# Kernel optimization log

Measured on AMD Instinct MI355X. Metric: run time of the kernel, lower is better.

The kernel has to match this reference:

```python
import jax, jax.numpy as jnp
import numpy as np

N_EMBD = 1024
BLOCK_SIZE = 2048
B = 8
LN_EPS = 1e-5


def _mlp(x, W1, b1, W2, b2):
    # Linear -> exact GELU -> Linear (torch nn.GELU default is erf-based)
    h = jax.nn.gelu(x @ W1 + b1, approximate=False)
    return h @ W2 + b2


def setup_inputs() -> dict:
    key = jax.random.key(0)
    ks = jax.random.split(key, 14)
    C = N_EMBD
    std = 0.02
    d = {"x": jax.random.normal(ks[0], (B, BLOCK_SIZE, C), dtype=jnp.float32)}
    names = ["q", "k", "v"]
    i = 1
    for n in names:
        d[f"W1{n}"] = jax.random.normal(ks[i], (C, C), dtype=jnp.float32) * std; i += 1
        d[f"b1{n}"] = jnp.zeros((C,), dtype=jnp.float32)
        d[f"W2{n}"] = jax.random.normal(ks[i], (C, C), dtype=jnp.float32) * std; i += 1
        d[f"b2{n}"] = jnp.zeros((C,), dtype=jnp.float32)
    d["ln_w"] = jnp.ones((C,), dtype=jnp.float32)
    d["ln_b"] = jnp.zeros((C,), dtype=jnp.float32)
    return d


def reference(x, W1q, b1q, W2q, b2q, W1k, b1k, W2k, b2k, W1v, b1v, W2v, b2v, ln_w, ln_b):
    Bsz, T, C = x.shape
    q = _mlp(x, W1q, b1q, W2q, b2q)
    k = _mlp(x, W1k, b1k, W2k, b2k)
    v = _mlp(x, W1v, b1v, W2v, b2v)
    scale = np.sqrt(N_EMBD * BLOCK_SIZE).astype(np.float32)
    scores = jnp.einsum("bid,bjd->bij", q, k) / scale  # [B,T,T]
    mask = jnp.tril(jnp.ones((T, T), dtype=scores.dtype))
    scores = scores * mask
    out = jnp.einsum("bij,bjd->bid", scores, v)  # [B,T,C]
    # LayerNorm with weight+bias, eps=1e-5
    mu = jnp.mean(out, axis=-1, keepdims=True)
    var = jnp.mean(jnp.square(out - mu), axis=-1, keepdims=True)
    out = (out - mu) * jax.lax.rsqrt(var + LN_EPS) * ln_w + ln_b
    return out
```

## Files before the change

### kernel.cpp

```cpp
#include <hip/hip_runtime.h>
#include <math.h>

#define BM 128
#define BN 128
#define BK 64

typedef _Float16 f16x8 __attribute__((ext_vector_type(8)));
typedef __attribute__((ext_vector_type(4))) float f32x4;

typedef const __attribute__((address_space(1))) void* gas_ptr;
typedef __attribute__((address_space(3))) void* las_ptr;

enum { OP_NONE = 0, OP_BIAS_GELU = 1, OP_BIAS = 2, OP_SCALE_MASK = 3 };

__device__ __forceinline__ unsigned short f2h(float f) {
    _Float16 h = (_Float16)f;
    unsigned short u;
    __builtin_memcpy(&u, &h, 2);
    return u;
}
__device__ __forceinline__ float h2f(unsigned short u) {
    _Float16 h;
    __builtin_memcpy(&h, &u, 2);
    return (float)h;
}

__device__ __forceinline__ float fast_gelu(float x) {
    float x2 = x * x;
    float p  = x * (-1.5957691216f - 0.0713548164f * x2);
    float t  = __expf(p);
    return x * __builtin_amdgcn_rcpf(1.0f + t);
}

template <int EPI, bool CAUSAL_K, bool TRI, bool REVM>
__global__ __launch_bounds__(256, 4) void gemm_bt(
    const unsigned short* __restrict__ A,
    const unsigned short* __restrict__ BT,
    unsigned short* __restrict__ Cw,
    const float* __restrict__ bias0,
    const float* __restrict__ bias1,
    const float* __restrict__ bias2,
    int M, int N, int K,
    long long sA, long long sB, long long sC,
    float scale)
{
    __shared__ __align__(16) unsigned short As[BM * BK];
    __shared__ __align__(16) unsigned short Bs[BN * BK];

    const int tid  = threadIdx.x;
    const int wave = tid >> 6;
    const int lane = tid & 63;

    int bm, bn, z;
    if (TRI) {
        const int t = blockIdx.x;
        int i = (int)((sqrtf(8.0f * t + 1.0f) - 1.0f) * 0.5f);
        while ((i + 1) * (i + 2) / 2 <= t) i++;
        while (i * (i + 1) / 2 > t) i--;
        const int j = t - i * (i + 1) / 2;
        bm = i * BM;
        bn = j * BN;
        z  = blockIdx.y;
    } else {
        bm = (REVM ? (gridDim.x - 1 - blockIdx.x) : blockIdx.x) * BM;
        bn = blockIdx.y * BN;
        z  = blockIdx.z;
    }

    const unsigned short* Ab = A  + (long long)z * sA;
    const unsigned short* Bb = BT + (long long)z * sB;
    unsigned short*       Cb = Cw + (long long)z * sC;
    const float* bias = nullptr;
    if (EPI == OP_BIAS || EPI == OP_BIAS_GELU)
        bias = (z == 0) ? bias0 : (z == 1) ? bias1 : bias2;

    const int wm = (wave >> 1) * 64;
    const int wn = (wave & 1) * 64;

    f32x4 acc[4][4];
    #pragma unroll
    for (int i = 0; i < 4; i++)
        #pragma unroll
        for (int j = 0; j < 4; j++)
            acc[i][j] = (f32x4){0.f, 0.f, 0.f, 0.f};

    int Keff = K;
    if (CAUSAL_K) {
        int kl = bm + BM;
        Keff = kl < K ? kl : K;
    }

    const int srow = lane >> 3;
    const int gchw = ((lane & 7) ^ (srow & 7)) * 8;
    const int fr   = lane & 15;
    const int quad = lane >> 4;

    const unsigned short* pA = Ab + (long long)(bm + wave * 32 + srow) * K + gchw;
    const unsigned short* pB = Bb + (long long)(bn + wave * 32 + srow) * K + gchw;
    const long long rstep = 8ll * K;

    for (int k0 = 0; k0 < Keff; k0 += BK) {
        #pragma unroll
        for (int s = 0; s < 4; ++s) {
            const int t = wave * 4 + s;
            __builtin_amdgcn_global_load_lds((gas_ptr)(const void*)(pA + s * rstep),
                                             (las_ptr)(void*)&As[t * 512 + lane * 8],
                                             16, 0, 0);
            __builtin_amdgcn_global_load_lds((gas_ptr)(const void*)(pB + s * rstep),
                                             (las_ptr)(void*)&Bs[t * 512 + lane * 8],
                                             16, 0, 0);
        }
        pA += BK;
        pB += BK;
        __syncthreads();

        #pragma unroll
        for (int kk = 0; kk < 2; ++kk) {
            f16x8 fa[4], fb[4];
            #pragma unroll
            for (int i = 0; i < 4; i++) {
                const int row  = wm + i * 16 + fr;
                const int slot = row * 8 + ((kk * 4 + quad) ^ (fr & 7));
                fa[i] = *(const f16x8*)&As[slot * 8];
            }
            #pragma unroll
            for (int j = 0; j < 4; j++) {
                const int row  = wn + j * 16 + fr;
                const int slot = row * 8 + ((kk * 4 + quad) ^ (fr & 7));
                fb[j] = *(const f16x8*)&Bs[slot * 8];
            }
            #pragma unroll
            for (int i = 0; i < 4; i++)
                #pragma unroll
                for (int j = 0; j < 4; j++)
                    acc[i][j] = __builtin_amdgcn_mfma_f32_16x16x32_f16(
                        fa[i], fb[j], acc[i][j], 0, 0, 0);
        }
        __syncthreads();
    }

    const int er = quad;
    const int ec = fr;
    #pragma unroll
    for (int j = 0; j < 4; j++) {
        const int col = bn + wn + j * 16 + ec;
        float bj = 0.f;
        if (EPI == OP_BIAS || EPI == OP_BIAS_GELU) bj = bias[col];
        #pragma unroll
        for (int i = 0; i < 4; i++) {
            #pragma unroll
            for (int r = 0; r < 4; r++) {
                const int row = bm + wm + i * 16 + er * 4 + r;
                float v = acc[i][j][r];
                if (EPI == OP_BIAS_GELU) {
                    v = fast_gelu(v + bj);
                } else if (EPI == OP_BIAS) {
                    v += bj;
                } else if (EPI == OP_SCALE_MASK) {
                    v *= scale;
                    if (col > row) v = 0.f;
                }
                Cb[(long long)row * N + col] = f2h(v);
            }
        }
    }
}

__global__ __launch_bounds__(256) void cvt_f32_f16(
    const float4* __restrict__ in, ushort4* __restrict__ out)
{
    int i = blockIdx.x * 256 + threadIdx.x;
    float4 f = in[i];
    ushort4 o;
    o.x = f2h(f.x); o.y = f2h(f.y); o.z = f2h(f.z); o.w = f2h(f.w);
    out[i] = o;
}

__global__ __launch_bounds__(256) void wprep(
    const float* __restrict__ s0, const float* __restrict__ s1,
    const float* __restrict__ s2, const float* __restrict__ s3,
    const float* __restrict__ s4, const float* __restrict__ s5,
    unsigned short* __restrict__ W1T, unsigned short* __restrict__ W2T)
{
    const int C = 1024;
    const int z = blockIdx.z;
    const float* in = (z == 0) ? s0 : (z == 1) ? s1 : (z == 2) ? s2
                    : (z == 3) ? s3 : (z == 4) ? s4 : s5;
    unsigned short* out = (z < 3) ? (W1T + (long long)z * C * C)
                                  : (W2T + (long long)(z - 3) * C * C);
    __shared__ unsigned short tile[32][33];
    const int bx = blockIdx.x * 32;
    const int by = blockIdx.y * 32;
    const int x = threadIdx.x;
    for (int y = threadIdx.y; y < 32; y += 8)
        tile[y][x] = f2h(in[(long long)(by + y) * C + (bx + x)]);
    __syncthreads();
    for (int y = threadIdx.y; y < 32; y += 8)
        out[(long long)(bx + y) * C + (by + x)] = tile[x][y];
}

__global__ __launch_bounds__(256) void transpose64_f16(
    const unsigned short* __restrict__ in,
    unsigned short* __restrict__ out,
    int rows, int cols,
    long long sIn, long long sOut)
{
    __shared__ unsigned short tile[64][68];
    const unsigned short* ip = in  + (long long)blockIdx.z * sIn;
    unsigned short*       op = out + (long long)blockIdx.z * sOut;
    const int bx = blockIdx.x * 64;
    const int by = blockIdx.y * 64;
    const int tid = threadIdx.x;
    const int rsub = tid >> 4;
    const int c4   = (tid & 15) * 4;
    #pragma unroll
    for (int it = 0; it < 4; it++) {
        const int r = it * 16 + rsub;
        ushort4 v = *(const ushort4*)&ip[(long long)(by + r) * cols + (bx + c4)];
        tile[r][c4]     = v.x;
        tile[r][c4 + 1] = v.y;
        tile[r][c4 + 2] = v.z;
        tile[r][c4 + 3] = v.w;
    }
    __syncthreads();
    #pragma unroll
    for (int it = 0; it < 4; it++) {
        const int cc = it * 16 + rsub;
        ushort4 v;
        v.x = tile[c4][cc];
        v.y = tile[c4 + 1][cc];
        v.z = tile[c4 + 2][cc];
        v.w = tile[c4 + 3][cc];
        *(ushort4*)&op[(long long)(bx + cc) * rows + (by + c4)] = v;
    }
}

__global__ __launch_bounds__(256) void layernorm_h(
    const unsigned short* __restrict__ X,
    const float* __restrict__ W,
    const float* __restrict__ Bv,
    float* __restrict__ Y)
{
    const int row = blockIdx.x;
    const int tid = threadIdx.x;
    ushort4 u = ((const ushort4*)(X + (long long)row * 1024))[tid];
    float f0 = h2f(u.x), f1 = h2f(u.y), f2 = h2f(u.z), f3 = h2f(u.w);
    float s  = f0 + f1 + f2 + f3;
    float ss = f0 * f0 + f1 * f1 + f2 * f2 + f3 * f3;
    #pragma unroll
    for (int off = 32; off > 0; off >>= 1) {
        s  += __shfl_down(s, off);
        ss += __shfl_down(ss, off);
    }
    __shared__ float red[2][4];
    const int wv = tid >> 6;
    if ((tid & 63) == 0) { red[0][wv] = s; red[1][wv] = ss; }
    __syncthreads();
    float S  = red[0][0] + red[0][1] + red[0][2] + red[0][3];
    float SS = red[1][0] + red[1][1] + red[1][2] + red[1][3];
    float mu  = S * (1.f / 1024.f);
    float var = SS * (1.f / 1024.f) - mu * mu;
    float rs  = rsqrtf(var + 1e-5f);
    float4 w4 = ((const float4*)W)[tid];
    float4 b4 = ((const float4*)Bv)[tid];
    float4 o;
    o.x = (f0 - mu) * rs * w4.x + b4.x;
    o.y = (f1 - mu) * rs * w4.y + b4.y;
    o.z = (f2 - mu) * rs * w4.z + b4.z;
    o.w = (f3 - mu) * rs * w4.w + b4.w;
    ((float4*)(Y + (long long)row * 1024))[tid] = o;
}

extern "C" void kernel_launch(void* const* d_in, const int* in_sizes, int n_in,
                              void* d_out, int out_size, void* d_ws, size_t ws_size,
                              hipStream_t stream)
{
    const int C  = 1024;
    const int T  = 2048;
    const int NB = 8;
    const int MT = NB * T;

    const float* x = (const float*)d_in[0];
    const float* W1q = (const float*)d_in[1];
    const float* b1q = (const float*)d_in[2];
    const float* W2q = (const float*)d_in[3];
    const float* b2q = (const float*)d_in[4];
    const float* W1k = (const float*)d_in[5];
    const float* b1k = (const float*)d_in[6];
    const float* W2k = (const float*)d_in[7];
    const float* b2k = (const float*)d_in[8];
    const float* W1v = (const float*)d_in[9];
    const float* b1v = (const float*)d_in[10];
    const float* W2v = (const float*)d_in[11];
    const float* b2v = (const float*)d_in[12];
    const float* lnw = (const float*)d_in[13];
    const float* lnb = (const float*)d_in[14];

    char* wsp = (char*)d_ws;
    auto take = [&](size_t bytes) {
        char* p = wsp;
        wsp += (bytes + 255) & ~(size_t)255;
        return p;
    };

    const size_t MATE = (size_t)MT * C;

    unsigned short* W1T  = (unsigned short*)take((size_t)3 * C * C * 2);
    unsigned short* W2T  = (unsigned short*)take((size_t)3 * C * C * 2);
    unsigned short* xb   = (unsigned short*)take(MATE * 2);
    unsigned short* qkv  = (unsigned short*)take(3 * MATE * 2);
    unsigned short* hreg = (unsigned short*)take(3 * MATE * 2);
    unsigned short* qb   = qkv;
    unsigned short* kb   = qkv + MATE;
    unsigned short* vb   = qkv + 2 * MATE;
    unsigned short* vT   = xb;
    unsigned short* scb  = hreg;
    unsigned short* opre = hreg + (size_t)NB * T * T;

    cvt_f32_f16<<<dim3(MT * C / 1024, 1, 1), dim3(256, 1, 1), 0, stream>>>(
        (const float4*)x, (ushort4*)xb);

    wprep<<<dim3(C / 32, C / 32, 6), dim3(32, 8, 1), 0, stream>>>(
        W1q, W1k, W1v, W2q, W2k, W2v, W1T, W2T);

    dim3 blk(256, 1, 1);

    gemm_bt<OP_BIAS_GELU, false, false, false><<<dim3(MT / BM, C / BN, 3), blk, 0, stream>>>(
        xb, W1T, hreg, b1q, b1k, b1v, MT, C, C,
        0, (long long)C * C, (long long)MATE, 1.f);

    gemm_bt<OP_BIAS, false, false, false><<<dim3(MT / BM, C / BN, 3), blk, 0, stream>>>(
        hreg, W2T, qkv, b2q, b2k, b2v, MT, C, C,
        (long long)MATE, (long long)C * C, (long long)MATE, 1.f);

    transpose64_f16<<<dim3(C / 64, T / 64, NB), blk, 0, stream>>>(
        vb, vT, T, C, (long long)T * C, (long long)T * C);

    float inv_scale = 1.0f / sqrtf((float)C * (float)T);
    gemm_bt<OP_SCALE_MASK, false, true, false><<<dim3(136, NB, 1), blk, 0, stream>>>(
        qb, kb, scb, nullptr, nullptr, nullptr, T, T, C,
        (long long)T * C, (long long)T * C, (long long)T * T, inv_scale);

    gemm_bt<OP_NONE, true, false, true><<<dim3(T / BM, C / BN, NB), blk, 0, stream>>>(
        scb, vT, opre, nullptr, nullptr, nullptr, T, C, T,
        (long long)T * T, (long long)T * C, (long long)T * C, 1.f);

    layernorm_h<<<dim3(MT, 1, 1), dim3(256, 1, 1), 0, stream>>>(
        opre, lnw, lnb, (float*)d_out);
}
```

Baseline: 553.0 us.

## Use 256x256 double-buffered GEMM kernel for the QKV MLP projections

Adds a new 512-thread GEMM kernel with 256x256 output tiles, double-buffered LDS filled via global_load_lds, XOR-swizzled LDS layout, and interleaved load/MFMA phases with priority hints. It replaces the 128x128 kernel for the two MLP GEMMs. The larger tile raises arithmetic intensity and the pipeline overlaps loads with MFMA work. The cost is higher LDS (128KB) and register pressure, which limits occupancy, and only 768 blocks per launch.

New measurement: 584.7 us. +5.7%, slower.

```diff
diff --git a/kernel.cpp b/kernel.cpp
--- a/kernel.cpp
+++ b/kernel.cpp
@@ -30,6 +30,179 @@
     float p  = x * (-1.5957691216f - 0.0713548164f * x2);
     float t  = __expf(p);
     return x * __builtin_amdgcn_rcpf(1.0f + t);
+}
+
+template <int EPI>
+__global__ __launch_bounds__(512, 2) void gemm256(
+    const unsigned short* __restrict__ A,
+    const unsigned short* __restrict__ BT,
+    unsigned short* __restrict__ Cw,
+    const float* __restrict__ bias0,
+    const float* __restrict__ bias1,
+    const float* __restrict__ bias2,
+    int M, int N, int K,
+    long long sA, long long sB, long long sC)
+{
+    __shared__ __align__(16) unsigned short As[2 * 256 * 64];
+    __shared__ __align__(16) unsigned short Bs[2 * 256 * 64];
+
+    const int tid  = threadIdx.x;
+    const int wave = tid >> 6;
+    const int lane = tid & 63;
+
+    const int bm = blockIdx.x * 256;
+    const int bn = blockIdx.y * 256;
+    const int z  = blockIdx.z;
+
+    const unsigned short* Ab = A  + (long long)z * sA;
+    const unsigned short* Bb = BT + (long long)z * sB;
+    unsigned short*       Cb = Cw + (long long)z * sC;
+    const float* bias = (z == 0) ? bias0 : (z == 1) ? bias1 : bias2;
+
+    const int wm = (wave >> 2) * 128;
+    const int wn = (wave & 3) * 64;
+
+    const int srow = lane >> 3;
+    const int swzc = (lane & 7) ^ srow;
+    const int fr   = lane & 15;
+    const int quad = lane >> 4;
+
+    const unsigned short* srcA = Ab + (long long)(bm + wave * 8 + srow) * K + swzc * 8;
+    const unsigned short* srcB = Bb + (long long)(bn + wave * 8 + srow) * K + swzc * 8;
+
+    const int NT = K >> 6;
+    const int NI = NT >> 1;
+
+    f32x4 acc[8][4];
+    #pragma unroll
+    for (int i = 0; i < 8; i++)
+        #pragma unroll
+        for (int j = 0; j < 4; j++)
+            acc[i][j] = (f32x4){0.f, 0.f, 0.f, 0.f};
+
+#define STG(src, lds, t, h)                                                    \
+    {                                                                          \
+        const int tc_ = ((t) < NT) ? (t) : ((t) & 1);                          \
+        const int bs_ = ((t) & 1) * 16384;                                     \
+        _Pragma("unroll")                                                      \
+        for (int s_ = 0; s_ < 2; ++s_) {                                       \
+            __builtin_amdgcn_global_load_lds(                                  \
+                (gas_ptr)(const void*)((src) +                                 \
+                    (long long)((h) * 128 + s_ * 64) * K + tc_ * 64),          \
+                (las_ptr)(void*)&lds[bs_ +                                     \
+                    ((h) * 128 + s_ * 64 + wave * 8) * 64 + lane * 8],         \
+                16, 0, 0);                                                     \
+        }                                                                      \
+    }
+
+#define LDA(d, q)                                                              \
+    _Pragma("unroll")                                                          \
+    for (int i_ = 0; i_ < 2; ++i_) {                                           \
+        _Pragma("unroll")                                                      \
+        for (int kk_ = 0; kk_ < 2; ++kk_) {                                    \
+            const int row_ = wm + (q) * 32 + i_ * 16 + fr;                     \
+            const int sl_  = row_ * 8 + ((kk_ * 4 + quad) ^ (row_ & 7));       \
+            fa[i_][kk_] = *(const f16x8*)&As[(d) * 16384 + sl_ * 8];           \
+        }                                                                      \
+    }
+
+#define LDB(d)                                                                 \
+    _Pragma("unroll")                                                          \
+    for (int j_ = 0; j_ < 4; ++j_) {                                           \
+        _Pragma("unroll")                                                      \
+        for (int kk_ = 0; kk_ < 2; ++kk_) {                                    \
+            const int row_ = wn + j_ * 16 + fr;                                \
+            const int sl_  = row_ * 8 + ((kk_ * 4 + quad) ^ (row_ & 7));       \
+            fb[j_][kk_] = *(const f16x8*)&Bs[(d) * 16384 + sl_ * 8];           \
+        }                                                                      \
+    }
+
+#define MFMAQ(q)                                                               \
+    __builtin_amdgcn_s_setprio(1);                                             \
+    _Pragma("unroll")                                                          \
+    for (int kk_ = 0; kk_ < 2; ++kk_) {                                        \
+        _Pragma("unroll")                                                      \
+        for (int i_ = 0; i_ < 2; ++i_) {                                       \
+            _Pragma("unroll")                                                  \
+            for (int j_ = 0; j_ < 4; ++j_) {                                   \
+                acc[(q) * 2 + i_][j_] = __builtin_amdgcn_mfma_f32_16x16x32_f16(\
+                    fa[i_][kk_], fb[j_][kk_], acc[(q) * 2 + i_][j_], 0, 0, 0); \
+            }                                                                  \
+        }                                                                      \
+    }                                                                          \
+    __builtin_amdgcn_s_setprio(0);
+
+#define SYNC1                                                                  \
+    __builtin_amdgcn_s_barrier();                                              \
+    asm volatile("s_waitcnt lgkmcnt(0)" ::: "memory");
+
+#define BAR2 __builtin_amdgcn_s_barrier();
+
+    STG(srcA, As, 0, 0); STG(srcA, As, 0, 1);
+    STG(srcB, Bs, 0, 0); STG(srcB, Bs, 0, 1);
+    STG(srcB, Bs, 1, 0); STG(srcB, Bs, 1, 1);
+    asm volatile("s_waitcnt vmcnt(4)" ::: "memory");
+    __builtin_amdgcn_s_barrier();
+
+    f16x8 fa[2][2], fb[4][2];
+
+    for (int it = 0; it < NI; ++it) {
+        const int t0 = it * 2;
+        LDB(0); LDA(0, 0);
+        STG(srcA, As, t0 + 1, 0);
+        SYNC1; MFMAQ(0); BAR2;
+        LDA(0, 1);
+        STG(srcA, As, t0 + 1, 1);
+        STG(srcB, Bs, t0 + 2, 0);
+        SYNC1; MFMAQ(1); BAR2;
+        LDA(0, 2);
+        STG(srcB, Bs, t0 + 2, 1);
+        SYNC1; MFMAQ(2); BAR2;
+        LDA(0, 3);
+        SYNC1; MFMAQ(3);
+        asm volatile("s_waitcnt vmcnt(4)" ::: "memory");
+        BAR2;
+        LDB(1); LDA(1, 0);
+        STG(srcA, As, t0 + 2, 0);
+        SYNC1; MFMAQ(0); BAR2;
+        LDA(1, 1);
+        STG(srcA, As, t0 + 2, 1);
+        STG(srcB, Bs, t0 + 3, 0);
+        SYNC1; MFMAQ(1); BAR2;
+        LDA(1, 2);
+        STG(srcB, Bs, t0 + 3, 1);
+        SYNC1; MFMAQ(2); BAR2;
+        LDA(1, 3);
+        SYNC1; MFMAQ(3);
+        asm volatile("s_waitcnt vmcnt(4)" ::: "memory");
+        BAR2;
+    }
+    asm volatile("s_waitcnt vmcnt(0)" ::: "memory");
+
+#undef STG
+#undef LDA
+#undef LDB
+#undef MFMAQ
+#undef SYNC1
+#undef BAR2
+
+    const int er = quad;
+    const int ec = fr;
+    #pragma unroll
+    for (int j = 0; j < 4; j++) {
+        const int col = bn + wn + j * 16 + ec;
+        const float bj = bias[col];
+        #pragma unroll
+        for (int i = 0; i < 8; i++) {
+            #pragma unroll
+            for (int r = 0; r < 4; r++) {
+                const int row = bm + wm + i * 16 + er * 4 + r;
+                float v = acc[i][j][r] + bj;
+                if (EPI == OP_BIAS_GELU) v = fast_gelu(v);
+                Cb[(long long)row * N + col] = f2h(v);
+            }
+        }
+    }
 }
 
 template <int EPI, bool CAUSAL_K, bool TRI, bool REVM>
@@ -324,14 +497,15 @@
         W1q, W1k, W1v, W2q, W2k, W2v, W1T, W2T);
 
     dim3 blk(256, 1, 1);
-
-    gemm_bt<OP_BIAS_GELU, false, false, false><<<dim3(MT / BM, C / BN, 3), blk, 0, stream>>>(
+    dim3 blk512(512, 1, 1);
+
+    gemm256<OP_BIAS_GELU><<<dim3(MT / 256, C / 256, 3), blk512, 0, stream>>>(
         xb, W1T, hreg, b1q, b1k, b1v, MT, C, C,
-        0, (long long)C * C, (long long)MATE, 1.f);
-
-    gemm_bt<OP_BIAS, false, false, false><<<dim3(MT / BM, C / BN, 3), blk, 0, stream>>>(
+        0, (long long)C * C, (long long)MATE);
+
+    gemm256<OP_BIAS><<<dim3(MT / 256, C / 256, 3), blk512, 0, stream>>>(
         hreg, W2T, qkv, b2q, b2k, b2v, MT, C, C,
-        (long long)MATE, (long long)C * C, (long long)MATE, 1.f);
+        (long long)MATE, (long long)C * C, (long long)MATE);
 
     transpose64_f16<<<dim3(C / 64, T / 64, NB), blk, 0, stream>>>(
         vb, vT, T, C, (long long)T * C, (long long)T * C);
```
